# Performance work log

Hardware: AMD Instinct MI355X
Metric: run time of the kernel (lower is better)

Reference implementation:

```python
import jax, jax.numpy as jnp
import numpy as np

D_MODEL = 1024
NUM_HEADS = 16
D_K = D_MODEL // NUM_HEADS


def setup_inputs() -> dict:
    key = jax.random.key(0)
    ks = jax.random.split(key, 9)
    s = 1.0 / np.sqrt(D_MODEL)
    X = jax.random.normal(ks[0], (4, 2048, D_MODEL), dtype=jnp.float32)
    Wq = jax.random.uniform(ks[1], (D_MODEL, D_MODEL), jnp.float32, -s, s)
    bq = jax.random.uniform(ks[2], (D_MODEL,), jnp.float32, -s, s)
    Wk = jax.random.uniform(ks[3], (D_MODEL, D_MODEL), jnp.float32, -s, s)
    bk = jax.random.uniform(ks[4], (D_MODEL,), jnp.float32, -s, s)
    Wv = jax.random.uniform(ks[5], (D_MODEL, D_MODEL), jnp.float32, -s, s)
    bv = jax.random.uniform(ks[6], (D_MODEL,), jnp.float32, -s, s)
    Wo = jax.random.uniform(ks[7], (D_MODEL, D_MODEL), jnp.float32, -s, s)
    bo = jax.random.uniform(ks[8], (D_MODEL,), jnp.float32, -s, s)
    return {"X": X, "Wq": Wq, "bq": bq, "Wk": Wk, "bk": bk,
            "Wv": Wv, "bv": bv, "Wo": Wo, "bo": bo}


def reference(X, Wq, bq, Wk, bk, Wv, bv, Wo, bo):
    B, n, d = X.shape
    # Linear layers: y = x @ W^T + b (torch Linear convention)
    Q = X @ Wq.T + bq
    K = X @ Wk.T + bk
    V = X @ Wv.T + bv
    # [B, n, H, d_k] -> [B, H, n, d_k]
    Q = Q.reshape(B, n, NUM_HEADS, D_K).transpose(0, 2, 1, 3)
    K = K.reshape(B, n, NUM_HEADS, D_K).transpose(0, 2, 1, 3)
    V = V.reshape(B, n, NUM_HEADS, D_K).transpose(0, 2, 1, 3)
    scores = jnp.einsum('bhqd,bhkd->bhqk', Q, K) / jnp.sqrt(jnp.float32(D_K))
    attn = jax.nn.softmax(scores, axis=-1)  # [B, H, n, n]
    out = jnp.einsum('bhqk,bhkd->bhqd', attn, V)
    out = out.transpose(0, 2, 1, 3).reshape(B, n, d)
    return out @ Wo.T + bo
```

## Files before the change

### kernel.cpp

```cpp
#include <hip/hip_runtime.h>
#include <hip/hip_bf16.h>
#include <stdint.h>

typedef __hip_bfloat16 bf16;
typedef __bf16 bf16x8 __attribute__((ext_vector_type(8)));
typedef float floatx4 __attribute__((ext_vector_type(4)));

#define MFMA16(a, b, c) __builtin_amdgcn_mfma_f32_16x16x32_bf16((a), (b), (c), 0, 0, 0)

typedef __attribute__((address_space(3))) uint32_t lds_u32;
typedef const __attribute__((address_space(1))) uint32_t gbl_u32;

__device__ __forceinline__ void async16(const void* g, void* s) {
    __builtin_amdgcn_global_load_lds((gbl_u32*)g, (lds_u32*)s, 16, 0, 0);
}

__device__ __forceinline__ unsigned short f2bf_rne(float f) {
    union { float f; unsigned u; } v; v.f = f;
    const unsigned u = v.u;
    return (unsigned short)((u + 0x7FFFu + ((u >> 16) & 1u)) >> 16);
}
__device__ __forceinline__ unsigned pk2(float a, float b) {
    __hip_bfloat162 h = __float22bfloat162_rn(make_float2(a, b));
    return *(unsigned*)&h;
}

#define A_X   0L
#define A_WQ  8388608L
#define A_WK  9437184L
#define A_WV  10485760L
#define A_WO  11534336L
#define A_END 12582912L

__global__ __launch_bounds__(256) void cvt5(
    const float* __restrict__ s0, const float* __restrict__ s1,
    const float* __restrict__ s2, const float* __restrict__ s3,
    const float* __restrict__ s4, unsigned short* __restrict__ dst)
{
    const long beg[6] = {A_X, A_WQ, A_WK, A_WV, A_WO, A_END};
    const float* srcs[5] = {s0, s1, s2, s3, s4};
    const long nchunk = A_END / 8;
    for (long c = (long)blockIdx.x * 256 + threadIdx.x; c < nchunk;
         c += (long)gridDim.x * 256) {
        const long off = c * 8;
        int s = 0;
#pragma unroll
        for (int i = 1; i < 5; ++i) if (off >= beg[i]) s = i;
        const float* sp = srcs[s] + (off - beg[s]);
        const uint4 lo = *(const uint4*)(sp);
        const uint4 hi = *(const uint4*)(sp + 4);
        const float* fl = (const float*)&lo;
        const float* fh = (const float*)&hi;
        uint4 o;
        o.x = pk2(fl[0], fl[1]); o.y = pk2(fl[2], fl[3]);
        o.z = pk2(fh[0], fh[1]); o.w = pk2(fh[2], fh[3]);
        *(uint4*)(dst + off) = o;
    }
}

template <int CFP32, int TRANSV>
__global__ __launch_bounds__(256, 2) void gemm_bt3(
    const bf16* __restrict__ A,
    const bf16* __restrict__ W0, const bf16* __restrict__ W1, const bf16* __restrict__ W2,
    const float* __restrict__ b0, const float* __restrict__ b1, const float* __restrict__ b2,
    void* __restrict__ C0, void* __restrict__ C1, void* __restrict__ C2)
{
    __shared__ bf16 As[128 * 64];
    __shared__ bf16 Bs[128 * 64];

    const int tid = threadIdx.x;
    const int which = blockIdx.y >> 3;
    const int nt = blockIdx.y & 7;
    const bf16* __restrict__ W   = (which == 0) ? W0 : ((which == 1) ? W1 : W2);
    const float* __restrict__ bb = (which == 0) ? b0 : ((which == 1) ? b1 : b2);
    void* __restrict__ C         = (which == 0) ? C0 : ((which == 1) ? C1 : C2);

    const int m0 = blockIdx.x * 128;
    const int n0 = nt * 128;

    const int w  = tid >> 6;
    const int l  = tid & 63;
    const int lr = l & 15;
    const int q  = l >> 4;
    const int wm = (w & 1) * 64;
    const int wn = (w >> 1) * 64;
    const int wbase = tid & 0xC0;

    floatx4 acc[4][4];
#pragma unroll
    for (int i = 0; i < 4; ++i)
#pragma unroll
        for (int j = 0; j < 4; ++j)
            acc[i][j] = (floatx4){0.f, 0.f, 0.f, 0.f};

#pragma unroll 1
    for (int kt = 0; kt < 16; ++kt) {
        __syncthreads();
#pragma unroll
        for (int r = 0; r < 4; ++r) {
            const int u   = r * 256 + tid;
            const int row = u >> 3;
            const int kg  = u & 7;
            const int kgg = kg ^ (row & 7);
            const size_t goffA = (size_t)(m0 + row) * 1024 + kt * 64 + kgg * 8;
            const size_t goffB = (size_t)(n0 + row) * 1024 + kt * 64 + kgg * 8;
            bf16* dA = As + (size_t)(r * 256 + wbase) * 8;
            bf16* dB = Bs + (size_t)(r * 256 + wbase) * 8;
            async16(A + goffA, dA);
            async16(W + goffB, dB);
        }
        asm volatile("s_waitcnt vmcnt(0)" ::: "memory");
        __syncthreads();

#pragma unroll
        for (int ks = 0; ks < 2; ++ks) {
            bf16x8 av[4], bv[4];
#pragma unroll
            for (int i = 0; i < 4; ++i) {
                const int row = wm + i * 16 + lr;
                const int kg  = (ks * 4 + q) ^ (row & 7);
                av[i] = *(const bf16x8*)(As + row * 64 + kg * 8);
            }
#pragma unroll
            for (int j = 0; j < 4; ++j) {
                const int row = wn + j * 16 + lr;
                const int kg  = (ks * 4 + q) ^ (row & 7);
                bv[j] = *(const bf16x8*)(Bs + row * 64 + kg * 8);
            }
#pragma unroll
            for (int i = 0; i < 4; ++i)
#pragma unroll
                for (int j = 0; j < 4; ++j)
                    acc[i][j] = MFMA16(av[i], bv[j], acc[i][j]);
        }
    }

    if (TRANSV && which == 2) {
#pragma unroll
        for (int j = 0; j < 4; ++j) {
            const int col = n0 + wn + j * 16 + lr;
            const float bj = bb[col];
            const int h = col >> 6, d = col & 63;
#pragma unroll
            for (int i = 0; i < 4; ++i) {
                const int row0 = m0 + wm + i * 16 + q * 4;
                const int b = row0 >> 11;
                const int key = row0 & 2047;
                uint2 ov;
                ov.x = pk2(acc[i][j][0] + bj, acc[i][j][1] + bj);
                ov.y = pk2(acc[i][j][2] + bj, acc[i][j][3] + bj);
                *(uint2*)((unsigned short*)C +
                          ((size_t)(b * 16 + h) * 64 + d) * 2048 + key) = ov;
            }
        }
    } else {
#pragma unroll
        for (int j = 0; j < 4; ++j) {
            const int col = n0 + wn + j * 16 + lr;
            const float bj = bb[col];
#pragma unroll
            for (int i = 0; i < 4; ++i) {
#pragma unroll
                for (int r = 0; r < 4; ++r) {
                    const int row = m0 + wm + i * 16 + q * 4 + r;
                    const float val = acc[i][j][r] + bj;
                    if (CFP32)
                        ((float*)C)[(long)row * 1024 + col] = val;
                    else
                        ((unsigned short*)C)[(long)row * 1024 + col] = f2bf_rne(val);
                }
            }
        }
    }
}

__device__ __forceinline__ int swzk(int R) {
    return (R & 7) ^ (((R >> 3) & 1) << 2);
}

__global__ __launch_bounds__(256, 2) void attn_flash(
    const bf16* __restrict__ Q, const bf16* __restrict__ K, const bf16* __restrict__ VT,
    bf16* __restrict__ AO)
{
    __shared__ bf16 Ks[2 * 64 * 64];
    __shared__ bf16 Vt[2 * 64 * 64];

    const int tid = threadIdx.x;
    const int b = blockIdx.y >> 4, h = blockIdx.y & 15;
    const int q0 = blockIdx.x * 128;
    const size_t base = ((size_t)b * 2048) * 1024 + (size_t)h * 64;
    const size_t vtb  = (size_t)(b * 16 + h) * 64 * 2048;

    const int w  = tid >> 6;
    const int l  = tid & 63;
    const int lr = l & 15;
    const int q  = l >> 4;

    const int krow = tid >> 3, kkg = tid & 7;
    const int vd = tid >> 2,   vko = tid & 3;
    const int ksw = kkg ^ swzk(krow);

    const int stK0 = krow * 64 + ksw * 8;
    const int stK1 = (32 + krow) * 64 + ksw * 8;
    const int stV0 = vd * 64 + ((vko ^ (vd & 7)) * 8);
    const int stV1 = vd * 64 + (((4 + vko) ^ (vd & 7)) * 8);

    bf16x8 qb[2][2];
#pragma unroll
    for (int i = 0; i < 2; ++i)
#pragma unroll
        for (int ks = 0; ks < 2; ++ks)
            qb[i][ks] = *(const bf16x8*)(Q + base +
                (size_t)(q0 + w * 32 + i * 16 + lr) * 1024 + ks * 32 + q * 8);

    uint4 kreg0 = *(const uint4*)(K + base + (size_t)krow * 1024 + kkg * 8);
    uint4 kreg1 = *(const uint4*)(K + base + (size_t)(32 + krow) * 1024 + kkg * 8);
    uint4 vreg0 = *(const uint4*)(VT + vtb + (size_t)vd * 2048 + vko * 8);
    uint4 vreg1 = *(const uint4*)(VT + vtb + (size_t)vd * 2048 + 32 + vko * 8);
    *(uint4*)(Ks + stK0) = kreg0;
    *(uint4*)(Ks + stK1) = kreg1;
    *(uint4*)(Vt + stV0) = vreg0;
    *(uint4*)(Vt + stV1) = vreg1;

    floatx4 O0[4], O1[4];
#pragma unroll
    for (int d = 0; d < 4; ++d) {
        O0[d] = (floatx4){0.f, 0.f, 0.f, 0.f};
        O1[d] = (floatx4){0.f, 0.f, 0.f, 0.f};
    }
    float m0 = -1e30f, m1 = -1e30f, ls0 = 0.f, ls1 = 0.f;
    const float cs = 0.18033688011112042f;

#pragma unroll 1
    for (int kt = 0; kt < 32; ++kt) {
        __syncthreads();
        const int bsel = (kt & 1) * 4096;
        const int bnxt = 4096 - bsel;

        const int ktn = (kt < 31) ? (kt + 1) : 31;
        const size_t kb_ = base + (size_t)ktn * 65536;
        kreg0 = *(const uint4*)(K + kb_ + (size_t)krow * 1024 + kkg * 8);
        kreg1 = *(const uint4*)(K + kb_ + (size_t)(32 + krow) * 1024 + kkg * 8);
        const size_t vb2 = vtb + (size_t)vd * 2048 + (size_t)ktn * 64;
        vreg0 = *(const uint4*)(VT + vb2 + vko * 8);
        vreg1 = *(const uint4*)(VT + vb2 + 32 + vko * 8);

        floatx4 s0[4], s1[4];
#pragma unroll
        for (int t = 0; t < 4; ++t) {
            s0[t] = (floatx4){0.f, 0.f, 0.f, 0.f};
            s1[t] = (floatx4){0.f, 0.f, 0.f, 0.f};
        }
#pragma unroll
        for (int ks = 0; ks < 2; ++ks) {
            bf16x8 kb[4];
#pragma unroll
            for (int t = 0; t < 4; ++t) {
                const int R = (t & 1) * 32 + (t >> 1) * 4 + (lr >> 2) * 8 + (lr & 3);
                kb[t] = *(const bf16x8*)(Ks + bsel + R * 64 +
                                         (((ks * 4 + q) ^ swzk(R)) * 8));
            }
            __builtin_amdgcn_s_setprio(1);
#pragma unroll
            for (int t = 0; t < 4; ++t) s0[t] = MFMA16(kb[t], qb[0][ks], s0[t]);
#pragma unroll
            for (int t = 0; t < 4; ++t) s1[t] = MFMA16(kb[t], qb[1][ks], s1[t]);
            __builtin_amdgcn_s_setprio(0);
        }

        float a0 = fmaxf(fmaxf(s0[0][0], s0[0][1]), s0[0][2]);
        float a1 = fmaxf(fmaxf(s0[0][3], s0[1][0]), s0[1][1]);
        float a2 = fmaxf(fmaxf(s0[1][2], s0[1][3]), s0[2][0]);
        float a3 = fmaxf(fmaxf(s0[2][1], s0[2][2]), s0[2][3]);
        float a4 = fmaxf(fmaxf(s0[3][0], s0[3][1]), s0[3][2]);
        const float mt0 = fmaxf(fmaxf(fmaxf(a0, a1), fmaxf(a2, a3)),
                                fmaxf(a4, s0[3][3])) * cs;
        float c0 = fmaxf(fmaxf(s1[0][0], s1[0][1]), s1[0][2]);
        float c1 = fmaxf(fmaxf(s1[0][3], s1[1][0]), s1[1][1]);
        float c2 = fmaxf(fmaxf(s1[1][2], s1[1][3]), s1[2][0]);
        float c3 = fmaxf(fmaxf(s1[2][1], s1[2][2]), s1[2][3]);
        float c4 = fmaxf(fmaxf(s1[3][0], s1[3][1]), s1[3][2]);
        const float mt1 = fmaxf(fmaxf(fmaxf(c0, c1), fmaxf(c2, c3)),
                                fmaxf(c4, s1[3][3])) * cs;

        if (__any((mt0 > m0 + 8.f) || (mt1 > m1 + 8.f))) {
            float vr0 = fmaxf(mt0, __shfl_xor(mt0, 16));
            vr0 = fmaxf(vr0, __shfl_xor(vr0, 32));
            const float mn0 = fmaxf(m0, vr0);
            const float al0 = __builtin_amdgcn_exp2f(m0 - mn0);
            m0 = mn0; ls0 *= al0;
#pragma unroll
            for (int d = 0; d < 4; ++d) O0[d] *= al0;
            float vr1 = fmaxf(mt1, __shfl_xor(mt1, 16));
            vr1 = fmaxf(vr1, __shfl_xor(vr1, 32));
            const float mn1 = fmaxf(m1, vr1);
            const float al1 = __builtin_amdgcn_exp2f(m1 - mn1);
            m1 = mn1; ls1 *= al1;
#pragma unroll
            for (int d = 0; d < 4; ++d) O1[d] *= al1;
        }

        bf16x8 va0[4];
#pragma unroll
        for (int dt = 0; dt < 4; ++dt) {
            const int R = dt * 16 + lr;
            va0[dt] = *(const bf16x8*)(Vt + bsel + R * 64 + ((q ^ (R & 7)) * 8));
        }

#pragma unroll
        for (int t = 0; t < 4; ++t)
#pragma unroll
            for (int r = 0; r < 4; ++r)
                s0[t][r] = __builtin_amdgcn_exp2f(s0[t][r] * cs - m0);
        {
            floatx4 rs = (s0[0] + s0[1]) + (s0[2] + s0[3]);
            ls0 += (rs[0] + rs[1]) + (rs[2] + rs[3]);
        }
        bf16x8 pb0[2];
#pragma unroll
        for (int kc = 0; kc < 2; ++kc) {
            union { uint4 u; bf16x8 v; } pw;
            pw.u.x = pk2(s0[kc][0], s0[kc][1]);
            pw.u.y = pk2(s0[kc][2], s0[kc][3]);
            pw.u.z = pk2(s0[kc + 2][0], s0[kc + 2][1]);
            pw.u.w = pk2(s0[kc + 2][2], s0[kc + 2][3]);
            pb0[kc] = pw.v;
        }

        __builtin_amdgcn_s_setprio(1);
#pragma unroll
        for (int dt = 0; dt < 4; ++dt) O0[dt] = MFMA16(va0[dt], pb0[0], O0[dt]);
        __builtin_amdgcn_s_setprio(0);

        bf16x8 va1[4];
#pragma unroll
        for (int dt = 0; dt < 4; ++dt) {
            const int R = dt * 16 + lr;
            va1[dt] = *(const bf16x8*)(Vt + bsel + R * 64 +
                                       (((4 + q) ^ (R & 7)) * 8));
        }

#pragma unroll
        for (int t = 0; t < 4; ++t)
#pragma unroll
            for (int r = 0; r < 4; ++r)
                s1[t][r] = __builtin_amdgcn_exp2f(s1[t][r] * cs - m1);
        {
            floatx4 rs = (s1[0] + s1[1]) + (s1[2] + s1[3]);
            ls1 += (rs[0] + rs[1]) + (rs[2] + rs[3]);
        }
        bf16x8 pb1[2];
#pragma unroll
        for (int kc = 0; kc < 2; ++kc) {
            union { uint4 u; bf16x8 v; } pw;
            pw.u.x = pk2(s1[kc][0], s1[kc][1]);
            pw.u.y = pk2(s1[kc][2], s1[kc][3]);
            pw.u.z = pk2(s1[kc + 2][0], s1[kc + 2][1]);
            pw.u.w = pk2(s1[kc + 2][2], s1[kc + 2][3]);
            pb1[kc] = pw.v;
        }

        __builtin_amdgcn_s_setprio(1);
#pragma unroll
        for (int dt = 0; dt < 4; ++dt) O0[dt] = MFMA16(va1[dt], pb0[1], O0[dt]);
#pragma unroll
        for (int dt = 0; dt < 4; ++dt) O1[dt] = MFMA16(va0[dt], pb1[0], O1[dt]);
#pragma unroll
        for (int dt = 0; dt < 4; ++dt) O1[dt] = MFMA16(va1[dt], pb1[1], O1[dt]);
        __builtin_amdgcn_s_setprio(0);

        *(uint4*)(Ks + bnxt + stK0) = kreg0;
        *(uint4*)(Ks + bnxt + stK1) = kreg1;
        *(uint4*)(Vt + bnxt + stV0) = vreg0;
        *(uint4*)(Vt + bnxt + stV1) = vreg1;
    }

    {
        float ls = ls0;
        ls += __shfl_xor(ls, 16);
        ls += __shfl_xor(ls, 32);
        const float inv = 1.f / ls;
        const int row = q0 + w * 32 + lr;
#pragma unroll
        for (int dt = 0; dt < 4; ++dt) {
            uint2 oh;
            oh.x = pk2(O0[dt][0] * inv, O0[dt][1] * inv);
            oh.y = pk2(O0[dt][2] * inv, O0[dt][3] * inv);
            *(uint2*)((unsigned short*)AO + base + (size_t)row * 1024 +
                      dt * 16 + q * 4) = oh;
        }
    }
    {
        float ls = ls1;
        ls += __shfl_xor(ls, 16);
        ls += __shfl_xor(ls, 32);
        const float inv = 1.f / ls;
        const int row = q0 + w * 32 + 16 + lr;
#pragma unroll
        for (int dt = 0; dt < 4; ++dt) {
            uint2 oh;
            oh.x = pk2(O1[dt][0] * inv, O1[dt][1] * inv);
            oh.y = pk2(O1[dt][2] * inv, O1[dt][3] * inv);
            *(uint2*)((unsigned short*)AO + base + (size_t)row * 1024 +
                      dt * 16 + q * 4) = oh;
        }
    }
}

extern "C" void kernel_launch(void* const* d_in, const int* in_sizes, int n_in,
                              void* d_out, int out_size, void* d_ws, size_t ws_size,
                              hipStream_t stream) {
    (void)in_sizes; (void)n_in; (void)out_size; (void)ws_size;
    const float* X  = (const float*)d_in[0];
    const float* Wq = (const float*)d_in[1];
    const float* bq = (const float*)d_in[2];
    const float* Wk = (const float*)d_in[3];
    const float* bk = (const float*)d_in[4];
    const float* Wv = (const float*)d_in[5];
    const float* bv = (const float*)d_in[6];
    const float* Wo = (const float*)d_in[7];
    const float* bo = (const float*)d_in[8];
    float* out = (float*)d_out;

    unsigned short* arena = (unsigned short*)d_ws;
    bf16* Xb  = (bf16*)(arena + A_X);
    bf16* Wqb = (bf16*)(arena + A_WQ);
    bf16* Wkb = (bf16*)(arena + A_WK);
    bf16* Wvb = (bf16*)(arena + A_WV);
    bf16* Wob = (bf16*)(arena + A_WO);

    const size_t SZ = (size_t)8192 * 1024;
    bf16* Qb  = (bf16*)(arena + A_END);
    bf16* Kb  = Qb + SZ;
    bf16* VTb = Kb + SZ;
    bf16* AOb = VTb + SZ;

    cvt5<<<dim3(1536), dim3(256), 0, stream>>>(X, Wq, Wk, Wv, Wo, arena);

    gemm_bt3<0, 1><<<dim3(64, 24), dim3(256), 0, stream>>>(
        Xb, Wqb, Wkb, Wvb, bq, bk, bv, (void*)Qb, (void*)Kb, (void*)VTb);

    attn_flash<<<dim3(16, 64), dim3(256), 0, stream>>>(Qb, Kb, VTb, AOb);

    gemm_bt3<1, 0><<<dim3(64, 8), dim3(256), 0, stream>>>(
        AOb, Wob, Wob, Wob, bo, bo, bo, (void*)out, (void*)out, (void*)out);
}
```

Measured before the change: 276.0 us.

## Use async global-to-LDS loads in attention and remap GEMM workgroup order

In the flash-attention kernel, the register-staged K/V prefetch (global load, then LDS store at the end of each iteration) is replaced by direct global_load_lds async copies into the next double buffer, with the swizzle moved to the source address. The barrier moves to the end of the loop after a vmcnt wait. This aims to free VGPRs and avoid the LDS write instructions. The change also keeps row sums as vector accumulators, reduced once at the end, loads both K halves before the QK MFMAs, and remaps the GEMM block index so consecutive workgroups are spread across XCDs for better L2 locality.

```diff
diff --git a/kernel.cpp b/kernel.cpp
--- a/kernel.cpp
+++ b/kernel.cpp
@@ -69,13 +69,19 @@
     __shared__ bf16 Bs[128 * 64];
 
     const int tid = threadIdx.x;
-    const int which = blockIdx.y >> 3;
-    const int nt = blockIdx.y & 7;
+    const int lin0 = blockIdx.y * 64 + blockIdx.x;
+    const int nwg  = gridDim.y << 6;
+    const int lin  = (lin0 & 7) * (nwg >> 3) + (lin0 >> 3);
+    const int bx = lin & 63;
+    const int by = lin >> 6;
+
+    const int which = by >> 3;
+    const int nt = by & 7;
     const bf16* __restrict__ W   = (which == 0) ? W0 : ((which == 1) ? W1 : W2);
     const float* __restrict__ bb = (which == 0) ? b0 : ((which == 1) ? b1 : b2);
     void* __restrict__ C         = (which == 0) ? C0 : ((which == 1) ? C1 : C2);
 
-    const int m0 = blockIdx.x * 128;
+    const int m0 = bx * 128;
     const int n0 = nt * 128;
 
     const int w  = tid >> 6;
@@ -196,14 +202,14 @@
     const int lr = l & 15;
     const int q  = l >> 4;
 
-    const int krow = tid >> 3, kkg = tid & 7;
-    const int vd = tid >> 2,   vko = tid & 3;
-    const int ksw = kkg ^ swzk(krow);
-
-    const int stK0 = krow * 64 + ksw * 8;
-    const int stK1 = (32 + krow) * 64 + ksw * 8;
-    const int stV0 = vd * 64 + ((vko ^ (vd & 7)) * 8);
-    const int stV1 = vd * 64 + (((4 + vko) ^ (vd & 7)) * 8);
+    const int srow = tid >> 3;
+    const int soct = tid & 7;
+    const int kr2  = 32 + srow;
+    const int kg1  = soct ^ swzk(srow);
+    const int kg2  = soct ^ swzk(kr2);
+    const int vg1  = soct ^ (srow & 7);
+    const int vg2  = soct ^ (kr2 & 7);
+    const int wch  = (tid & 0xC0) * 8;
 
     bf16x8 qb[2][2];
 #pragma unroll
@@ -213,60 +219,58 @@
             qb[i][ks] = *(const bf16x8*)(Q + base +
                 (size_t)(q0 + w * 32 + i * 16 + lr) * 1024 + ks * 32 + q * 8);
 
-    uint4 kreg0 = *(const uint4*)(K + base + (size_t)krow * 1024 + kkg * 8);
-    uint4 kreg1 = *(const uint4*)(K + base + (size_t)(32 + krow) * 1024 + kkg * 8);
-    uint4 vreg0 = *(const uint4*)(VT + vtb + (size_t)vd * 2048 + vko * 8);
-    uint4 vreg1 = *(const uint4*)(VT + vtb + (size_t)vd * 2048 + 32 + vko * 8);
-    *(uint4*)(Ks + stK0) = kreg0;
-    *(uint4*)(Ks + stK1) = kreg1;
-    *(uint4*)(Vt + stV0) = vreg0;
-    *(uint4*)(Vt + stV1) = vreg1;
-
+    {
+        const bf16* kp = K + base;
+        async16(kp + (size_t)srow * 1024 + kg1 * 8, Ks + wch);
+        async16(kp + (size_t)kr2 * 1024 + kg2 * 8,  Ks + 2048 + wch);
+        const bf16* vp = VT + vtb;
+        async16(vp + (size_t)srow * 2048 + vg1 * 8, Vt + wch);
+        async16(vp + (size_t)kr2 * 2048 + vg2 * 8,  Vt + 2048 + wch);
+    }
+    asm volatile("s_waitcnt vmcnt(0)" ::: "memory");
+    __syncthreads();
+
+    const floatx4 z4 = (floatx4){0.f, 0.f, 0.f, 0.f};
     floatx4 O0[4], O1[4];
 #pragma unroll
-    for (int d = 0; d < 4; ++d) {
-        O0[d] = (floatx4){0.f, 0.f, 0.f, 0.f};
-        O1[d] = (floatx4){0.f, 0.f, 0.f, 0.f};
-    }
-    float m0 = -1e30f, m1 = -1e30f, ls0 = 0.f, ls1 = 0.f;
+    for (int d = 0; d < 4; ++d) { O0[d] = z4; O1[d] = z4; }
+    float m0 = -1e30f, m1 = -1e30f;
+    floatx4 ls0v = z4, ls1v = z4;
     const float cs = 0.18033688011112042f;
 
 #pragma unroll 1
     for (int kt = 0; kt < 32; ++kt) {
-        __syncthreads();
         const int bsel = (kt & 1) * 4096;
         const int bnxt = 4096 - bsel;
 
         const int ktn = (kt < 31) ? (kt + 1) : 31;
-        const size_t kb_ = base + (size_t)ktn * 65536;
-        kreg0 = *(const uint4*)(K + kb_ + (size_t)krow * 1024 + kkg * 8);
-        kreg1 = *(const uint4*)(K + kb_ + (size_t)(32 + krow) * 1024 + kkg * 8);
-        const size_t vb2 = vtb + (size_t)vd * 2048 + (size_t)ktn * 64;
-        vreg0 = *(const uint4*)(VT + vb2 + vko * 8);
-        vreg1 = *(const uint4*)(VT + vb2 + 32 + vko * 8);
-
+        {
+            const bf16* kp = K + base + (size_t)ktn * 65536;
+            async16(kp + (size_t)srow * 1024 + kg1 * 8, Ks + bnxt + wch);
+            async16(kp + (size_t)kr2 * 1024 + kg2 * 8,  Ks + bnxt + 2048 + wch);
+            const bf16* vp = VT + vtb + (size_t)ktn * 64;
+            async16(vp + (size_t)srow * 2048 + vg1 * 8, Vt + bnxt + wch);
+            async16(vp + (size_t)kr2 * 2048 + vg2 * 8,  Vt + bnxt + 2048 + wch);
+        }
+
+        bf16x8 kb0[4], kb1[4];
+#pragma unroll
+        for (int t = 0; t < 4; ++t) {
+            const int R = (t & 1) * 32 + (t >> 1) * 4 + (lr >> 2) * 8 + (lr & 3);
+            kb0[t] = *(const bf16x8*)(Ks + bsel + R * 64 + ((q ^ swzk(R)) * 8));
+            kb1[t] = *(const bf16x8*)(Ks + bsel + R * 64 + (((4 + q) ^ swzk(R)) * 8));
+        }
         floatx4 s0[4], s1[4];
-#pragma unroll
-        for (int t = 0; t < 4; ++t) {
-            s0[t] = (floatx4){0.f, 0.f, 0.f, 0.f};
-            s1[t] = (floatx4){0.f, 0.f, 0.f, 0.f};
-        }
-#pragma unroll
-        for (int ks = 0; ks < 2; ++ks) {
-            bf16x8 kb[4];
-#pragma unroll
-            for (int t = 0; t < 4; ++t) {
-                const int R = (t & 1) * 32 + (t >> 1) * 4 + (lr >> 2) * 8 + (lr & 3);
-                kb[t] = *(const bf16x8*)(Ks + bsel + R * 64 +
-                                         (((ks * 4 + q) ^ swzk(R)) * 8));
-            }
-            __builtin_amdgcn_s_setprio(1);
-#pragma unroll
-            for (int t = 0; t < 4; ++t) s0[t] = MFMA16(kb[t], qb[0][ks], s0[t]);
-#pragma unroll
-            for (int t = 0; t < 4; ++t) s1[t] = MFMA16(kb[t], qb[1][ks], s1[t]);
-            __builtin_amdgcn_s_setprio(0);
-        }
+        __builtin_amdgcn_s_setprio(1);
+#pragma unroll
+        for (int t = 0; t < 4; ++t) s0[t] = MFMA16(kb0[t], qb[0][0], z4);
+#pragma unroll
+        for (int t = 0; t < 4; ++t) s0[t] = MFMA16(kb1[t], qb[0][1], s0[t]);
+#pragma unroll
+        for (int t = 0; t < 4; ++t) s1[t] = MFMA16(kb0[t], qb[1][0], z4);
+#pragma unroll
+        for (int t = 0; t < 4; ++t) s1[t] = MFMA16(kb1[t], qb[1][1], s1[t]);
+        __builtin_amdgcn_s_setprio(0);
 
         float a0 = fmaxf(fmaxf(s0[0][0], s0[0][1]), s0[0][2]);
         float a1 = fmaxf(fmaxf(s0[0][3], s0[1][0]), s0[1][1]);
@@ -288,14 +292,14 @@
             vr0 = fmaxf(vr0, __shfl_xor(vr0, 32));
             const float mn0 = fmaxf(m0, vr0);
             const float al0 = __builtin_amdgcn_exp2f(m0 - mn0);
-            m0 = mn0; ls0 *= al0;
+            m0 = mn0; ls0v *= al0;
 #pragma unroll
             for (int d = 0; d < 4; ++d) O0[d] *= al0;
             float vr1 = fmaxf(mt1, __shfl_xor(mt1, 16));
             vr1 = fmaxf(vr1, __shfl_xor(vr1, 32));
             const float mn1 = fmaxf(m1, vr1);
             const float al1 = __builtin_amdgcn_exp2f(m1 - mn1);
-            m1 = mn1; ls1 *= al1;
+            m1 = mn1; ls1v *= al1;
 #pragma unroll
             for (int d = 0; d < 4; ++d) O1[d] *= al1;
         }
@@ -312,10 +316,7 @@
 #pragma unroll
             for (int r = 0; r < 4; ++r)
                 s0[t][r] = __builtin_amdgcn_exp2f(s0[t][r] * cs - m0);
-        {
-            floatx4 rs = (s0[0] + s0[1]) + (s0[2] + s0[3]);
-            ls0 += (rs[0] + rs[1]) + (rs[2] + rs[3]);
-        }
+        ls0v += (s0[0] + s0[1]) + (s0[2] + s0[3]);
         bf16x8 pb0[2];
 #pragma unroll
         for (int kc = 0; kc < 2; ++kc) {
@@ -345,10 +346,7 @@
 #pragma unroll
             for (int r = 0; r < 4; ++r)
                 s1[t][r] = __builtin_amdgcn_exp2f(s1[t][r] * cs - m1);
-        {
-            floatx4 rs = (s1[0] + s1[1]) + (s1[2] + s1[3]);
-            ls1 += (rs[0] + rs[1]) + (rs[2] + rs[3]);
-        }
+        ls1v += (s1[0] + s1[1]) + (s1[2] + s1[3]);
         bf16x8 pb1[2];
 #pragma unroll
         for (int kc = 0; kc < 2; ++kc) {
@@ -369,14 +367,12 @@
         for (int dt = 0; dt < 4; ++dt) O1[dt] = MFMA16(va1[dt], pb1[1], O1[dt]);
         __builtin_amdgcn_s_setprio(0);
 
-        *(uint4*)(Ks + bnxt + stK0) = kreg0;
-        *(uint4*)(Ks + bnxt + stK1) = kreg1;
-        *(uint4*)(Vt + bnxt + stV0) = vreg0;
-        *(uint4*)(Vt + bnxt + stV1) = vreg1;
+        asm volatile("s_waitcnt vmcnt(0)" ::: "memory");
+        __syncthreads();
     }
 
     {
-        float ls = ls0;
+        float ls = (ls0v[0] + ls0v[1]) + (ls0v[2] + ls0v[3]);
         ls += __shfl_xor(ls, 16);
         ls += __shfl_xor(ls, 32);
         const float inv = 1.f / ls;
@@ -391,7 +387,7 @@
         }
     }
     {
-        float ls = ls1;
+        float ls = (ls1v[0] + ls1v[1]) + (ls1v[2] + ls1v[3]);
         ls += __shfl_xor(ls, 16);
         ls += __shfl_xor(ls, 32);
         const float inv = 1.f / ls;
```

After: 302.4 us. 9.6% more time.
